# Kernel optimization log

Measured on AMD Instinct MI355X. Metric: run time of the kernel, lower is better.

Reference implementation:

```python
import jax, jax.numpy as jnp
import numpy as np

LN_EPS = 1e-5  # torch nn.LayerNorm default eps


def _layernorm(x, g, b):
    m = jnp.mean(x, -1, keepdims=True)
    v = jnp.mean((x - m) ** 2, -1, keepdims=True)
    return (x - m) / jnp.sqrt(v + LN_EPS) * g + b


def _dw_causal_conv(x, w, bias=None):
    # x: (B, L, C); w: (C, K) depthwise kernels; causal via left-pad K-1
    C = x.shape[-1]
    K = w.shape[-1]
    xt = jnp.swapaxes(x, 1, 2)                       # (B, C, L)
    xp = jnp.pad(xt, ((0, 0), (0, 0), (K - 1, 0)))
    y = jax.lax.conv_general_dilated(
        xp, w[:, None, :], (1,), 'VALID',
        feature_group_count=C, dimension_numbers=('NCH', 'OIH', 'NCH'))
    if bias is not None:
        y = y + bias[None, :, None]
    return jnp.swapaxes(y, 1, 2)                     # (B, L, C)


def _s4d(x, Bp, Cp, log_dt, Dp):
    # Diagonal SSM: kernel K[l] = sum_n C[n]*dB[n]*dA[n]^l, shared across channels
    L, Dm = x.shape[1], x.shape[2]
    n = Bp.shape[0]
    A = -jnp.arange(1, n + 1, dtype=x.dtype)
    dt = jnp.clip(jnp.exp(log_dt), 1e-4, 1.0)
    dA = jnp.exp(jnp.clip(dt * A, -10.0, 10.0))                  # (n,)
    dB = (dA - 1.0) / jnp.minimum(A, -1e-4) * Bp                 # (n,)
    pows = dA[:, None] ** jnp.arange(L, dtype=x.dtype)[None, :]  # (n, L)
    Kk = jnp.nan_to_num((Cp * dB) @ pows, nan=0.0, posinf=0.0, neginf=0.0)  # (L,)
    y = _dw_causal_conv(x, jnp.broadcast_to(Kk[None, :], (Dm, L)))
    return y + Dp * x


def _mamba_block(x, g, b, W_in, cw, cb, sB, sC, ldt, sD, W_out, rs):
    res = x
    h = _layernorm(x, g, b)
    xz = h @ W_in.T                                  # (B, L, 2*d_inner)
    xp, z = jnp.split(xz, 2, axis=-1)
    xc = _dw_causal_conv(xp, cw, cb)                 # depthwise causal conv, k=4
    y = _s4d(xc, sB, sC, ldt, sD) * jax.nn.sigmoid(z)
    y = y @ W_out.T
    return res + jnp.clip(rs, 0.0, 1.5) * y          # dropout is identity in eval


def _forward(spatial_tokens_init, pos_embed, ln_g, ln_b, W_in, conv_w, conv_b,
             ssm_B, ssm_C, log_dt, ssm_D, W_out, res_scale, fin_g, fin_b,
             imp_W1, imp_b1, imp_W2, imp_b2, tex_W, tex_b, edge_W, edge_b,
             str_W, str_b):
    x = spatial_tokens_init + pos_embed
    for i in range(ln_g.shape[0]):  # fixed small layer count
        x = _mamba_block(x, ln_g[i], ln_b[i], W_in[i], conv_w[i], conv_b[i],
                         ssm_B[i], ssm_C[i], log_dt[i], ssm_D[i], W_out[i],
                         res_scale[i])
    tokens = _layernorm(x, fin_g, fin_b)
    # F.normalize(dim=-1, eps=1e-6)
    tn = tokens / jnp.maximum(jnp.sqrt(jnp.sum(tokens ** 2, -1, keepdims=True)), 1e-6)
    h = jax.nn.gelu(tn @ imp_W1.T + imp_b1, approximate=False)
    logits = (h @ imp_W2.T + imp_b2)[..., 0]
    w = jax.nn.softmax(logits, axis=-1)
    feats = jnp.sum(tokens * w[..., None], axis=1)
    return (feats,
            feats @ tex_W.T + tex_b,
            feats @ edge_W.T + edge_b,
            feats @ str_W.T + str_b,
            tokens, w)


B, N, D, DI, NL, NS, KC, DH = 512, 256, 128, 256, 4, 16, 4, 64
H = D // 2


def setup_inputs() -> dict:
    ks = jax.random.split(jax.random.key(0), 26)
    r = lambda k, sh, s=0.02: jax.random.normal(k, sh, dtype=jnp.float32) * s
    inp = {
        'spatial_tokens_init': jax.random.normal(ks[0], (B, N, D), dtype=jnp.float32),
        'pos_embed': r(ks[1], (1, N, D)),
        'ln_g': jnp.ones((NL, D), jnp.float32),
        'ln_b': jnp.zeros((NL, D), jnp.float32),
        'W_in': r(ks[2], (NL, 2 * DI, D)),
        'conv_w': r(ks[3], (NL, DI, KC), 0.2),
        'conv_b': r(ks[4], (NL, DI), 0.02),
        'ssm_B': r(ks[5], (NL, NS)),
        'ssm_C': r(ks[6], (NL, NS)),
        'log_dt': jax.random.uniform(ks[7], (NL,), jnp.float32,
                                     minval=float(np.log(1e-3)), maxval=float(np.log(0.1))),
        'ssm_D': jnp.zeros((NL,), jnp.float32),
        'W_out': r(ks[8], (NL, D, DI)),
        'res_scale': jnp.ones((NL,), jnp.float32),
        'fin_g': jnp.ones((D,), jnp.float32),
        'fin_b': jnp.zeros((D,), jnp.float32),
        'imp_W1': r(ks[9], (H, D)),
        'imp_b1': jnp.zeros((H,), jnp.float32),
        'imp_W2': r(ks[10], (1, H)),
        'imp_b2': jnp.zeros((1,), jnp.float32),
        'tex_W': r(ks[11], (DH, D)),
        'tex_b': jnp.zeros((DH,), jnp.float32),
        'edge_W': r(ks[12], (DH, D)),
        'edge_b': jnp.zeros((DH,), jnp.float32),
        'str_W': r(ks[13], (DH, D)),
        'str_b': jnp.zeros((DH,), jnp.float32),
    }
    return inp


def reference(spatial_tokens_init, pos_embed, ln_g, ln_b, W_in, conv_w, conv_b,
              ssm_B, ssm_C, log_dt, ssm_D, W_out, res_scale, fin_g, fin_b,
              imp_W1, imp_b1, imp_W2, imp_b2, tex_W, tex_b, edge_W, edge_b,
              str_W, str_b):
    return _forward(spatial_tokens_init, pos_embed, ln_g, ln_b, W_in, conv_w,
                    conv_b, ssm_B, ssm_C, log_dt, ssm_D, W_out, res_scale,
                    fin_g, fin_b, imp_W1, imp_b1, imp_W2, imp_b2, tex_W, tex_b,
                    edge_W, edge_b, str_W, str_b)
```

## Files before the change

### kernel.cpp

```cpp
#include <hip/hip_runtime.h>
#include <hip/hip_bf16.h>


typedef __bf16 bf16_8 __attribute__((ext_vector_type(8)));
typedef __bf16 bf16_4 __attribute__((ext_vector_type(4)));
typedef float  f32_4  __attribute__((ext_vector_type(4)));

#define GLOAD16(src, dst) __builtin_amdgcn_global_load_lds( \
    (const __attribute__((address_space(1))) void*)(src),   \
    (__attribute__((address_space(3))) void*)(dst), 16, 0, 0)

__device__ __forceinline__ float fsig(float z) {
    float e = __expf(-z);
    return __builtin_amdgcn_rcpf(1.0f + e);
}

__global__ __launch_bounds__(256) void prep_kernel(const float* __restrict__ win,
                                                   const float* __restrict__ wout,
                                                   const float* __restrict__ w1,
                                                   __bf16* __restrict__ win16,
                                                   __bf16* __restrict__ wout16,
                                                   __bf16* __restrict__ w116) {
    int i = blockIdx.x * 256 + threadIdx.x;
    if (i < 4 * 512 * 128) win16[i] = (__bf16)win[i];
    if (i < 4 * 128 * 256) wout16[i] = (__bf16)wout[i];
    if (i < 64 * 128)      w116[i]  = (__bf16)w1[i];
}

__global__ __launch_bounds__(256) void build_T_kernel(const float* __restrict__ Bp,
                                                      const float* __restrict__ Cp,
                                                      const float* __restrict__ ldt,
                                                      const float* __restrict__ Dpv,
                                                      __bf16* __restrict__ Tg,
                                                      float* __restrict__ Rg) {
    __shared__ float rsum[4];
    int layer = blockIdx.y, l = blockIdx.x, j = threadIdx.x;
    int d = l - j;
    float val = 0.0f;
    if (d >= 0) {
        float dt = expf(ldt[layer]);
        dt = fminf(fmaxf(dt, 1e-4f), 1.0f);
        #pragma unroll
        for (int n = 0; n < 16; ++n) {
            float A = -(float)(n + 1);
            float e = fminf(fmaxf(dt * A, -10.0f), 10.0f);
            float dA = expf(e);
            float dB = (dA - 1.0f) / A * Bp[layer * 16 + n];
            val += Cp[layer * 16 + n] * dB * expf(e * (float)d);
        }
        if (d == 0) val += Dpv[layer];
    }
    __bf16 bv = (__bf16)val;
    Tg[layer * 65536 + l * 256 + j] = bv;
    float fv = (float)bv;
    #pragma unroll
    for (int o = 32; o; o >>= 1) fv += __shfl_xor(fv, o);
    int lane = j & 63, wave = j >> 6;
    if (lane == 0) rsum[wave] = fv;
    __syncthreads();
    if (j == 0) Rg[layer * 256 + l] = rsum[0] + rsum[1] + rsum[2] + rsum[3];
}

__global__ __launch_bounds__(256) void ln_first_kernel(const float4* __restrict__ init4,
                                                       const float4* __restrict__ pos4,
                                                       const float* __restrict__ g,
                                                       const float* __restrict__ bta,
                                                       __bf16* __restrict__ x,
                                                       __bf16* __restrict__ h) {
    int tid = threadIdx.x;
    int wave = tid >> 6, lane = tid & 63;
    int half = lane >> 5, l32 = lane & 31;
    long tok = (long)blockIdx.x * 8 + wave * 2 + half;
    float4 v = init4[tok * 32 + l32];
    float4 p = pos4[(tok & 255) * 32 + l32];
    v.x += p.x; v.y += p.y; v.z += p.z; v.w += p.w;
    int d0 = l32 * 4;
    bf16_4 xv;
    xv[0] = (__bf16)v.x; xv[1] = (__bf16)v.y; xv[2] = (__bf16)v.z; xv[3] = (__bf16)v.w;
    *(bf16_4*)(x + tok * 128 + d0) = xv;
    float s = v.x + v.y + v.z + v.w;
    float ss = v.x * v.x + v.y * v.y + v.z * v.z + v.w * v.w;
    #pragma unroll
    for (int o = 16; o; o >>= 1) { s += __shfl_xor(s, o); ss += __shfl_xor(ss, o); }
    float m = s * (1.0f / 128.0f);
    float var = ss * (1.0f / 128.0f) - m * m;
    float r = rsqrtf(var + 1e-5f);
    bf16_4 hv;
    hv[0] = (__bf16)((v.x - m) * r * g[d0]     + bta[d0]);
    hv[1] = (__bf16)((v.y - m) * r * g[d0 + 1] + bta[d0 + 1]);
    hv[2] = (__bf16)((v.z - m) * r * g[d0 + 2] + bta[d0 + 2]);
    hv[3] = (__bf16)((v.w - m) * r * g[d0 + 3] + bta[d0 + 3]);
    *(bf16_4*)(h + tok * 128 + d0) = hv;
}

__global__ __launch_bounds__(256) void gemm1_kernel(const __bf16* __restrict__ hmat,
                                                    const __bf16* __restrict__ win,
                                                    __bf16* __restrict__ xpt,
                                                    __bf16* __restrict__ z) {
    __shared__ __align__(16) __bf16 As[128 * 64];
    __shared__ __align__(16) __bf16 Bs[128 * 64];
    int tid = threadIdx.x;
    int bid = blockIdx.x;
    long m0 = (long)((bid & 7) + ((bid >> 5) << 3)) * 128;
    int n0 = ((bid >> 3) & 3) * 128;
    int wave = tid >> 6, lane = tid & 63;
    int wm = wave >> 1, wn = wave & 1;
    int lrow = lane & 15, lk = (lane >> 4) * 8;
    int r7 = lrow & 7;
    int rl = lane >> 3, sl = lane & 7;
    int scol = ((sl ^ rl) << 3);
    f32_4 acc[4][4] = {};

    for (int kc = 0; kc < 2; ++kc) {
        const __bf16* asrc = hmat + m0 * 128 + kc * 64;
        const __bf16* bsrc = win + (long)n0 * 128 + kc * 64;
        #pragma unroll
        for (int j = 0; j < 4; ++j) {
            int chunk = wave * 4 + j;
            GLOAD16(asrc + (long)(chunk * 8 + rl) * 128 + scol, As + chunk * 512);
            GLOAD16(bsrc + (long)(chunk * 8 + rl) * 128 + scol, Bs + chunk * 512);
        }
        __syncthreads();
        #pragma unroll
        for (int kk = 0; kk < 64; kk += 32) {
            int sw = ((((kk + lk) >> 3) ^ r7) << 3);
            bf16_8 a[4], b[4];
            #pragma unroll
            for (int mt = 0; mt < 4; ++mt)
                a[mt] = *(const bf16_8*)(As + (wm * 64 + mt * 16 + lrow) * 64 + sw);
            #pragma unroll
            for (int nt = 0; nt < 4; ++nt)
                b[nt] = *(const bf16_8*)(Bs + (wn * 64 + nt * 16 + lrow) * 64 + sw);
            #pragma unroll
            for (int mt = 0; mt < 4; ++mt)
                #pragma unroll
                for (int nt = 0; nt < 4; ++nt)
                    acc[mt][nt] = __builtin_amdgcn_mfma_f32_16x16x32_bf16(
                        a[mt], b[nt], acc[mt][nt], 0, 0, 0);
        }
        __syncthreads();
    }

    int row_base = (lane >> 4) * 4;
    int col = lane & 15;
    if (n0 < 256) {
        #pragma unroll
        for (int mt = 0; mt < 4; ++mt) {
            long mg = m0 + wm * 64 + mt * 16 + row_base;
            int b = (int)(mg >> 8), l = (int)(mg & 255);
            #pragma unroll
            for (int nt = 0; nt < 4; ++nt) {
                int ng = n0 + wn * 64 + nt * 16 + col;
                bf16_4 o;
                #pragma unroll
                for (int r = 0; r < 4; ++r) o[r] = (__bf16)acc[mt][nt][r];
                *(bf16_4*)(xpt + (long)b * 65536 + (long)ng * 256 + l) = o;
            }
        }
    } else {
        int ncol0 = n0 - 256;
        #pragma unroll
        for (int mt = 0; mt < 4; ++mt) {
            long mg = m0 + wm * 64 + mt * 16 + row_base;
            #pragma unroll
            for (int nt = 0; nt < 4; ++nt) {
                int ng = ncol0 + wn * 64 + nt * 16 + col;
                #pragma unroll
                for (int r = 0; r < 4; ++r)
                    z[(mg + r) * 256 + ng] = (__bf16)acc[mt][nt][r];
            }
        }
    }
}

__global__ __launch_bounds__(512) void ssm_gemm_kernel(const __bf16* __restrict__ xct,
                                                       __bf16* __restrict__ zy,
                                                       const __bf16* __restrict__ Tg,
                                                       const float* __restrict__ Rg,
                                                       const float* __restrict__ cw,
                                                       const float* __restrict__ cb) {
    __shared__ __align__(16) __bf16 As[256 * 64];
    __shared__ __align__(16) __bf16 Bs[128 * 64];
    __shared__ float  bnd[3][128];
    __shared__ float  Rs[256];
    int tid = threadIdx.x;
    int batch = blockIdx.x >> 1;
    int ntile = blockIdx.x & 1;
    int c0 = ntile * 128;

    int wave = tid >> 6, lane = tid & 63;
    int wm = wave >> 2, wn = wave & 3;
    int lrow = lane & 15, lk = (lane >> 4) * 8;
    int r7 = lrow & 7;
    int quad = lane >> 4;
    int rl = lane >> 3, sl = lane & 7;
    int scol = ((sl ^ rl) << 3);
    f32_4 acc[8][2] = {};
    const __bf16* bsrc0 = xct + (long)batch * 65536 + (long)c0 * 256;

    if (tid < 256) Rs[tid] = Rg[tid];

    for (int kc = 0; kc < 4; ++kc) {
        int j0 = kc * 64;
        const __bf16* asrc = Tg + j0;
        const __bf16* bsrc = bsrc0 + j0;
        #pragma unroll
        for (int j = 0; j < 4; ++j) {
            int chunk = wave * 4 + j;
            GLOAD16(asrc + (long)(chunk * 8 + rl) * 256 + scol, As + chunk * 512);
        }
        #pragma unroll
        for (int j = 0; j < 2; ++j) {
            int chunk = wave * 2 + j;
            GLOAD16(bsrc + (long)(chunk * 8 + rl) * 256 + scol, Bs + chunk * 512);
        }
        __syncthreads();
        #pragma unroll
        for (int kk = 0; kk < 64; kk += 32) {
            int sw = ((((kk + lk) >> 3) ^ r7) << 3);
            bf16_8 b0 = *(const bf16_8*)(Bs + (wn * 32 + lrow) * 64 + sw);
            bf16_8 b1 = *(const bf16_8*)(Bs + (wn * 32 + 16 + lrow) * 64 + sw);
            #pragma unroll
            for (int mt = 0; mt < 8; ++mt) {
                bf16_8 a = *(const bf16_8*)(As + (wm * 128 + mt * 16 + lrow) * 64 + sw);
                acc[mt][0] = __builtin_amdgcn_mfma_f32_16x16x32_bf16(a, b0, acc[mt][0], 0, 0, 0);
                acc[mt][1] = __builtin_amdgcn_mfma_f32_16x16x32_bf16(a, b1, acc[mt][1], 0, 0, 0);
            }
        }
        __syncthreads();
    }

    if (wm == 0 && quad == 3) {
        #pragma unroll
        for (int nt = 0; nt < 2; ++nt) {
            int colb = wn * 32 + nt * 16 + lrow;
            bnd[0][colb] = acc[7][nt][1];
            bnd[1][colb] = acc[7][nt][2];
            bnd[2][colb] = acc[7][nt][3];
        }
    }
    __syncthreads();

    float4 wv[2]; float cbv[2];
    #pragma unroll
    for (int nt = 0; nt < 2; ++nt) {
        int cg = c0 + wn * 32 + nt * 16 + lrow;
        wv[nt] = *(const float4*)(cw + cg * 4);
        cbv[nt] = cb[cg];
    }
    int src = (lane + 48) & 63;

    #pragma unroll
    for (int mt = 0; mt < 8; ++mt) {
        int lbase = wm * 128 + mt * 16 + quad * 4;
        int mp = mt > 0 ? mt - 1 : 0;
        float R0 = Rs[lbase], R1 = Rs[lbase + 1], R2 = Rs[lbase + 2], R3 = Rs[lbase + 3];
        #pragma unroll
        for (int nt = 0; nt < 2; ++nt) {
            int colb = wn * 32 + nt * 16 + lrow;
            int cg = c0 + colb;
            float s1 = __shfl(acc[mt][nt][3], src);
            float s2 = __shfl(acc[mt][nt][2], src);
            float s3 = __shfl(acc[mt][nt][1], src);
            float t1, t2, t3;
            if (mt == 0) {
                if (wm == 1) { t1 = bnd[2][colb]; t2 = bnd[1][colb]; t3 = bnd[0][colb]; }
                else         { t1 = 0.0f; t2 = 0.0f; t3 = 0.0f; }
            } else {
                t1 = __shfl(acc[mp][nt][3], src);
                t2 = __shfl(acc[mp][nt][2], src);
                t3 = __shfl(acc[mp][nt][1], src);
            }
            float pm1 = quad ? s1 : t1;
            float pm2 = quad ? s2 : t2;
            float pm3 = quad ? s3 : t3;
            float p0 = acc[mt][nt][0], p1 = acc[mt][nt][1];
            float p2 = acc[mt][nt][2], p3 = acc[mt][nt][3];
            float y0 = wv[nt].x * pm3 + wv[nt].y * pm2 + wv[nt].z * pm1 + wv[nt].w * p0 + cbv[nt] * R0;
            float y1 = wv[nt].x * pm2 + wv[nt].y * pm1 + wv[nt].z * p0  + wv[nt].w * p1 + cbv[nt] * R1;
            float y2 = wv[nt].x * pm1 + wv[nt].y * p0  + wv[nt].z * p1  + wv[nt].w * p2 + cbv[nt] * R2;
            float y3 = wv[nt].x * p0  + wv[nt].y * p1  + wv[nt].z * p2  + wv[nt].w * p3 + cbv[nt] * R3;
            long base = (long)batch * 65536 + (long)lbase * 256 + cg;
            float z0 = (float)zy[base];
            float z1 = (float)zy[base + 256];
            float z2 = (float)zy[base + 512];
            float z3 = (float)zy[base + 768];
            zy[base]       = (__bf16)(y0 * fsig(z0));
            zy[base + 256] = (__bf16)(y1 * fsig(z1));
            zy[base + 512] = (__bf16)(y2 * fsig(z2));
            zy[base + 768] = (__bf16)(y3 * fsig(z3));
        }
    }
}

__global__ __launch_bounds__(256) void gemm2_kernel(const __bf16* __restrict__ y,
                                                    const __bf16* __restrict__ wout,
                                                    __bf16* __restrict__ x,
                                                    const float* __restrict__ rs_p,
                                                    const float* __restrict__ g,
                                                    const float* __restrict__ bta,
                                                    __bf16* __restrict__ hout,
                                                    float* __restrict__ tokens_out,
                                                    int final_mode) {
    __shared__ __align__(16) __bf16 As[64 * 64];
    __shared__ __align__(16) __bf16 Bs[128 * 64];
    __shared__ float s_sum[64][2];
    __shared__ float s_ssq[64][2];
    int tid = threadIdx.x;
    long m0 = (long)blockIdx.x * 64;
    int wave = tid >> 6, lane = tid & 63;
    int wm = wave >> 1, wn = wave & 1;
    int lrow = lane & 15, lk = (lane >> 4) * 8;
    int r7 = lrow & 7;
    int rl = lane >> 3, sl = lane & 7;
    int scol = ((sl ^ rl) << 3);
    f32_4 acc[2][4] = {};

    for (int kc = 0; kc < 4; ++kc) {
        const __bf16* asrc = y + m0 * 256 + kc * 64;
        const __bf16* bsrc = wout + kc * 64;
        #pragma unroll
        for (int j = 0; j < 2; ++j) {
            int chunk = wave * 2 + j;
            GLOAD16(asrc + (long)(chunk * 8 + rl) * 256 + scol, As + chunk * 512);
        }
        #pragma unroll
        for (int j = 0; j < 4; ++j) {
            int chunk = wave * 4 + j;
            GLOAD16(bsrc + (long)(chunk * 8 + rl) * 256 + scol, Bs + chunk * 512);
        }
        __syncthreads();
        #pragma unroll
        for (int kk = 0; kk < 64; kk += 32) {
            int sw = ((((kk + lk) >> 3) ^ r7) << 3);
            bf16_8 a[2], b[4];
            #pragma unroll
            for (int mt = 0; mt < 2; ++mt)
                a[mt] = *(const bf16_8*)(As + (wm * 32 + mt * 16 + lrow) * 64 + sw);
            #pragma unroll
            for (int nt = 0; nt < 4; ++nt)
                b[nt] = *(const bf16_8*)(Bs + (wn * 64 + nt * 16 + lrow) * 64 + sw);
            #pragma unroll
            for (int mt = 0; mt < 2; ++mt)
                #pragma unroll
                for (int nt = 0; nt < 4; ++nt)
                    acc[mt][nt] = __builtin_amdgcn_mfma_f32_16x16x32_bf16(
                        a[mt], b[nt], acc[mt][nt], 0, 0, 0);
        }
        __syncthreads();
    }

    float rs = rs_p[0];
    rs = fminf(fmaxf(rs, 0.0f), 1.5f);
    int quad = lane >> 4;
    int col = lane & 15;

    #pragma unroll
    for (int mt = 0; mt < 2; ++mt) {
        int tb = wm * 32 + mt * 16 + quad * 4;
        long mg = m0 + tb;
        #pragma unroll
        for (int r = 0; r < 4; ++r) {
            float s = 0.0f, ss = 0.0f;
            #pragma unroll
            for (int nt = 0; nt < 4; ++nt) {
                int d = wn * 64 + nt * 16 + col;
                float xv = (float)x[(mg + r) * 128 + d] + rs * acc[mt][nt][r];
                acc[mt][nt][r] = xv;
                s += xv; ss += xv * xv;
            }
            #pragma unroll
            for (int o = 8; o; o >>= 1) { s += __shfl_xor(s, o); ss += __shfl_xor(ss, o); }
            if (col == 0) {
                s_sum[tb + r][wn] = s;
                s_ssq[tb + r][wn] = ss;
            }
        }
    }
    __syncthreads();

    #pragma unroll
    for (int mt = 0; mt < 2; ++mt) {
        int tb = wm * 32 + mt * 16 + quad * 4;
        long mg = m0 + tb;
        #pragma unroll
        for (int r = 0; r < 4; ++r) {
            float s  = s_sum[tb + r][0] + s_sum[tb + r][1];
            float ss = s_ssq[tb + r][0] + s_ssq[tb + r][1];
            float m = s * (1.0f / 128.0f);
            float var = ss * (1.0f / 128.0f) - m * m;
            float rstd = rsqrtf(var + 1e-5f);
            #pragma unroll
            for (int nt = 0; nt < 4; ++nt) {
                int d = wn * 64 + nt * 16 + col;
                float xv = acc[mt][nt][r];
                float t = (xv - m) * rstd * g[d] + bta[d];
                if (!final_mode) {
                    x[(mg + r) * 128 + d] = (__bf16)xv;
                    hout[(mg + r) * 128 + d] = (__bf16)t;
                } else {
                    tokens_out[(mg + r) * 128 + d] = t;
                }
            }
        }
    }
}

__global__ __launch_bounds__(256) void l2n_kernel(const float4* __restrict__ tokens4,
                                                  __bf16* __restrict__ tn) {
    int tid = threadIdx.x;
    int wave = tid >> 6, lane = tid & 63;
    int half = lane >> 5, l32 = lane & 31;
    long tok = (long)blockIdx.x * 8 + wave * 2 + half;
    float4 t = tokens4[tok * 32 + l32];
    float q = t.x * t.x + t.y * t.y + t.z * t.z + t.w * t.w;
    #pragma unroll
    for (int o = 16; o; o >>= 1) q += __shfl_xor(q, o);
    float inv = 1.0f / fmaxf(sqrtf(q), 1e-6f);
    bf16_4 o4;
    o4[0] = (__bf16)(t.x * inv); o4[1] = (__bf16)(t.y * inv);
    o4[2] = (__bf16)(t.z * inv); o4[3] = (__bf16)(t.w * inv);
    *(bf16_4*)(tn + tok * 128 + l32 * 4) = o4;
}

#define LDA 136
__global__ __launch_bounds__(256) void mlp_kernel(const __bf16* __restrict__ tn,
                                                  const __bf16* __restrict__ w1b,
                                                  const float* __restrict__ b1,
                                                  const float* __restrict__ W2,
                                                  const float* __restrict__ b2,
                                                  float* __restrict__ logits) {
    __shared__ __bf16 As[128 * LDA];
    __shared__ __bf16 Bs[64 * LDA];
    int tid = threadIdx.x;
    long m0 = (long)blockIdx.x * 128;
    const __bf16* asrc = tn + m0 * 128;
    #pragma unroll
    for (int i = 0; i < 8; ++i) {
        int idx = tid + i * 256;
        int row = idx >> 4, c = idx & 15;
        uint4 v = *(const uint4*)(asrc + row * 128 + c * 8);
        *(uint4*)(As + row * LDA + c * 8) = v;
    }
    #pragma unroll
    for (int i = 0; i < 4; ++i) {
        int idx = tid + i * 256;
        int row = idx >> 4, c = idx & 15;
        uint4 v = *(const uint4*)(w1b + row * 128 + c * 8);
        *(uint4*)(Bs + row * LDA + c * 8) = v;
    }
    __syncthreads();

    int wave = tid >> 6, lane = tid & 63;
    int lrow = lane & 15, lk = (lane >> 4) * 8;
    f32_4 acc[2][4] = {};
    #pragma unroll
    for (int kk = 0; kk < 128; kk += 32) {
        bf16_8 a[2], b[4];
        #pragma unroll
        for (int mt = 0; mt < 2; ++mt)
            a[mt] = *(const bf16_8*)(As + (wave * 32 + mt * 16 + lrow) * LDA + kk + lk);
        #pragma unroll
        for (int nt = 0; nt < 4; ++nt)
            b[nt] = *(const bf16_8*)(Bs + (nt * 16 + lrow) * LDA + kk + lk);
        #pragma unroll
        for (int mt = 0; mt < 2; ++mt)
            #pragma unroll
            for (int nt = 0; nt < 4; ++nt)
                acc[mt][nt] = __builtin_amdgcn_mfma_f32_16x16x32_bf16(
                    a[mt], b[nt], acc[mt][nt], 0, 0, 0);
    }

    int col = lane & 15, quad = lane >> 4;
    float b2v = b2[0];
    #pragma unroll
    for (int mt = 0; mt < 2; ++mt) {
        #pragma unroll
        for (int r = 0; r < 4; ++r) {
            float p = 0.0f;
            #pragma unroll
            for (int nt = 0; nt < 4; ++nt) {
                int jx = nt * 16 + col;
                float a = acc[mt][nt][r] + b1[jx];
                float gl = 0.5f * a * (1.0f + erff(a * 0.70710678118654752f));
                p += gl * W2[jx];
            }
            #pragma unroll
            for (int o = 8; o; o >>= 1) p += __shfl_xor(p, o);
            if (col == 0) {
                long tok = m0 + wave * 32 + mt * 16 + quad * 4 + r;
                logits[tok] = p + b2v;
            }
        }
    }
}

__global__ __launch_bounds__(256) void head_kernel(const float* __restrict__ tokens,
                                                   const float* __restrict__ logits,
                                                   const float* __restrict__ texW,
                                                   const float* __restrict__ texb,
                                                   const float* __restrict__ edgeW,
                                                   const float* __restrict__ edgeb,
                                                   const float* __restrict__ strW,
                                                   const float* __restrict__ strb,
                                                   float* __restrict__ feats_out,
                                                   float* __restrict__ tex_out,
                                                   float* __restrict__ edge_out,
                                                   float* __restrict__ str_out,
                                                   float* __restrict__ w_out) {
    __shared__ float wsm[256];
    __shared__ float red[8];
    __shared__ float feats_s[128];
    int b = blockIdx.x, tid = threadIdx.x;
    int lane = tid & 63, wave = tid >> 6;
    float lg = logits[(long)b * 256 + tid];
    float mx = lg;
    #pragma unroll
    for (int o = 32; o; o >>= 1) mx = fmaxf(mx, __shfl_xor(mx, o));
    if (lane == 0) red[wave] = mx;
    __syncthreads();
    float bm = fmaxf(fmaxf(red[0], red[1]), fmaxf(red[2], red[3]));
    float e = expf(lg - bm);
    float se = e;
    #pragma unroll
    for (int o = 32; o; o >>= 1) se += __shfl_xor(se, o);
    if (lane == 0) red[4 + wave] = se;
    __syncthreads();
    float tot = red[4] + red[5] + red[6] + red[7];
    float w = e / tot;
    wsm[tid] = w;
    w_out[(long)b * 256 + tid] = w;
    __syncthreads();
    if (tid < 128) {
        float acc = 0.0f;
        const float* tb = tokens + (long)b * 256 * 128 + tid;
        #pragma unroll 4
        for (int l = 0; l < 256; ++l) acc += tb[l * 128] * wsm[l];
        feats_s[tid] = acc;
        feats_out[(long)b * 128 + tid] = acc;
    }
    __syncthreads();
    if (tid < 192) {
        int head = tid >> 6, j = tid & 63;
        const float* W  = head == 0 ? texW : (head == 1 ? edgeW : strW);
        const float* bi = head == 0 ? texb : (head == 1 ? edgeb : strb);
        float* outp     = head == 0 ? tex_out : (head == 1 ? edge_out : str_out);
        const float* wr = W + j * 128;
        float acc = 0.0f;
        #pragma unroll 8
        for (int k = 0; k < 128; ++k) acc += feats_s[k] * wr[k];
        outp[(long)b * 64 + j] = acc + bi[j];
    }
}

extern "C" void kernel_launch(void* const* d_in, const int* in_sizes, int n_in,
                              void* d_out, int out_size, void* d_ws, size_t ws_size,
                              hipStream_t stream) {
    const float* init   = (const float*)d_in[0];
    const float* pos    = (const float*)d_in[1];
    const float* ln_g   = (const float*)d_in[2];
    const float* ln_b   = (const float*)d_in[3];
    const float* W_in   = (const float*)d_in[4];
    const float* conv_w = (const float*)d_in[5];
    const float* conv_b = (const float*)d_in[6];
    const float* ssm_B  = (const float*)d_in[7];
    const float* ssm_C  = (const float*)d_in[8];
    const float* log_dt = (const float*)d_in[9];
    const float* ssm_D  = (const float*)d_in[10];
    const float* W_out  = (const float*)d_in[11];
    const float* res_sc = (const float*)d_in[12];
    const float* fin_g  = (const float*)d_in[13];
    const float* fin_b  = (const float*)d_in[14];
    const float* imp_W1 = (const float*)d_in[15];
    const float* imp_b1 = (const float*)d_in[16];
    const float* imp_W2 = (const float*)d_in[17];
    const float* imp_b2 = (const float*)d_in[18];
    const float* tex_W  = (const float*)d_in[19];
    const float* tex_b  = (const float*)d_in[20];
    const float* edge_W = (const float*)d_in[21];
    const float* edge_b = (const float*)d_in[22];
    const float* str_W  = (const float*)d_in[23];
    const float* str_b  = (const float*)d_in[24];

    float* out = (float*)d_out;
    char* ws = (char*)d_ws;
    __bf16* x      = (__bf16*)ws;
    __bf16* xpt    = (__bf16*)(ws + 67108864);
    __bf16* zb     = (__bf16*)(ws + 134217728);
    __bf16* hb     = (__bf16*)(ws + 201326592);
    __bf16* win16  = (__bf16*)(ws + 234881024);
    __bf16* wout16 = (__bf16*)(ws + 235405312);
    float*  logits = (float*)(ws + 235667456);
    __bf16* w1b    = (__bf16*)(ws + 236191744);
    __bf16* Tg     = (__bf16*)(ws + 236208128);
    float*  Rg     = (float*)(ws + 236732416);

    float* tokens = out + 163840;

    prep_kernel<<<1024, 256, 0, stream>>>(W_in, W_out, imp_W1, win16, wout16, w1b);
    build_T_kernel<<<dim3(256, 4), 256, 0, stream>>>(ssm_B, ssm_C, log_dt, ssm_D, Tg, Rg);
    ln_first_kernel<<<16384, 256, 0, stream>>>((const float4*)init, (const float4*)pos,
                                               ln_g, ln_b, x, hb);
    for (int l = 0; l < 4; ++l) {
        gemm1_kernel<<<4096, 256, 0, stream>>>(hb, win16 + l * 65536, xpt, zb);
        ssm_gemm_kernel<<<1024, 512, 0, stream>>>(xpt, zb, Tg + l * 65536, Rg + l * 256,
                                                  conv_w + l * 1024, conv_b + l * 256);
        int fin = (l == 3);
        const float* gn = fin ? fin_g : ln_g + (l + 1) * 128;
        const float* bn = fin ? fin_b : ln_b + (l + 1) * 128;
        gemm2_kernel<<<2048, 256, 0, stream>>>(zb, wout16 + l * 32768, x, res_sc + l,
                                               gn, bn, hb, fin ? tokens : nullptr, fin);
    }
    __bf16* tn = hb;
    l2n_kernel<<<16384, 256, 0, stream>>>((const float4*)tokens, tn);
    mlp_kernel<<<1024, 256, 0, stream>>>(tn, w1b, imp_b1, imp_W2, imp_b2, logits);
    head_kernel<<<512, 256, 0, stream>>>(tokens, logits, tex_W, tex_b, edge_W, edge_b,
                                         str_W, str_b, out, out + 65536, out + 98304,
                                         out + 131072, out + 16941056);
}
```

Before: 697.8 us.

## Compute z gate inside SSM kernel instead of materializing it in gemm1

Gemm1 now produces only the xp half of the input projection. The SSM kernel recomputes the z half for its own 256x128 tile with an extra MFMA pass over h and W_in, and keeps it in registers. The sigmoid gating then reads z directly from those accumulators. This removes the z write and read round-trip through global memory and halves the gemm1 grid. The cost is an additional 16x2 accumulator array in the SSM kernel, which raises register pressure and may reduce occupancy.

```diff
diff --git a/kernel.cpp b/kernel.cpp
--- a/kernel.cpp
+++ b/kernel.cpp
@@ -95,14 +95,13 @@
 
 __global__ __launch_bounds__(256) void gemm1_kernel(const __bf16* __restrict__ hmat,
                                                     const __bf16* __restrict__ win,
-                                                    __bf16* __restrict__ xpt,
-                                                    __bf16* __restrict__ z) {
+                                                    __bf16* __restrict__ xpt) {
     __shared__ __align__(16) __bf16 As[128 * 64];
     __shared__ __align__(16) __bf16 Bs[128 * 64];
     int tid = threadIdx.x;
     int bid = blockIdx.x;
-    long m0 = (long)((bid & 7) + ((bid >> 5) << 3)) * 128;
-    int n0 = ((bid >> 3) & 3) * 128;
+    long m0 = (long)((bid & 7) + ((bid >> 4) << 3)) * 128;
+    int n0 = ((bid >> 3) & 1) * 128;
     int wave = tid >> 6, lane = tid & 63;
     int wm = wave >> 1, wn = wave & 1;
     int lrow = lane & 15, lk = (lane >> 4) * 8;
@@ -143,38 +142,25 @@
 
     int row_base = (lane >> 4) * 4;
     int col = lane & 15;
-    if (n0 < 256) {
-        #pragma unroll
-        for (int mt = 0; mt < 4; ++mt) {
-            long mg = m0 + wm * 64 + mt * 16 + row_base;
-            int b = (int)(mg >> 8), l = (int)(mg & 255);
-            #pragma unroll
-            for (int nt = 0; nt < 4; ++nt) {
-                int ng = n0 + wn * 64 + nt * 16 + col;
-                bf16_4 o;
-                #pragma unroll
-                for (int r = 0; r < 4; ++r) o[r] = (__bf16)acc[mt][nt][r];
-                *(bf16_4*)(xpt + (long)b * 65536 + (long)ng * 256 + l) = o;
-            }
-        }
-    } else {
-        int ncol0 = n0 - 256;
-        #pragma unroll
-        for (int mt = 0; mt < 4; ++mt) {
-            long mg = m0 + wm * 64 + mt * 16 + row_base;
-            #pragma unroll
-            for (int nt = 0; nt < 4; ++nt) {
-                int ng = ncol0 + wn * 64 + nt * 16 + col;
-                #pragma unroll
-                for (int r = 0; r < 4; ++r)
-                    z[(mg + r) * 256 + ng] = (__bf16)acc[mt][nt][r];
-            }
+    #pragma unroll
+    for (int mt = 0; mt < 4; ++mt) {
+        long mg = m0 + wm * 64 + mt * 16 + row_base;
+        int b = (int)(mg >> 8), l = (int)(mg & 255);
+        #pragma unroll
+        for (int nt = 0; nt < 4; ++nt) {
+            int ng = n0 + wn * 64 + nt * 16 + col;
+            bf16_4 o;
+            #pragma unroll
+            for (int r = 0; r < 4; ++r) o[r] = (__bf16)acc[mt][nt][r];
+            *(bf16_4*)(xpt + (long)b * 65536 + (long)ng * 256 + l) = o;
         }
     }
 }
 
 __global__ __launch_bounds__(512) void ssm_gemm_kernel(const __bf16* __restrict__ xct,
-                                                       __bf16* __restrict__ zy,
+                                                       const __bf16* __restrict__ hmat,
+                                                       const __bf16* __restrict__ winz,
+                                                       __bf16* __restrict__ yb,
                                                        const __bf16* __restrict__ Tg,
                                                        const float* __restrict__ Rg,
                                                        const float* __restrict__ cw,
@@ -196,10 +182,40 @@
     int rl = lane >> 3, sl = lane & 7;
     int scol = ((sl ^ rl) << 3);
     f32_4 acc[8][2] = {};
+    f32_4 accz[8][2] = {};
+
+    if (tid < 256) Rs[tid] = Rg[tid];
+
+    const __bf16* hsrc0 = hmat + (long)batch * 32768;
+    for (int kc = 0; kc < 2; ++kc) {
+        int j0 = kc * 64;
+        #pragma unroll
+        for (int j = 0; j < 4; ++j) {
+            int chunk = wave * 4 + j;
+            GLOAD16(hsrc0 + (long)(chunk * 8 + rl) * 128 + j0 + scol, As + chunk * 512);
+        }
+        #pragma unroll
+        for (int j = 0; j < 2; ++j) {
+            int chunk = wave * 2 + j;
+            GLOAD16(winz + (long)(c0 + chunk * 8 + rl) * 128 + j0 + scol, Bs + chunk * 512);
+        }
+        __syncthreads();
+        #pragma unroll
+        for (int kk = 0; kk < 64; kk += 32) {
+            int sw = ((((kk + lk) >> 3) ^ r7) << 3);
+            bf16_8 b0 = *(const bf16_8*)(Bs + (wn * 32 + lrow) * 64 + sw);
+            bf16_8 b1 = *(const bf16_8*)(Bs + (wn * 32 + 16 + lrow) * 64 + sw);
+            #pragma unroll
+            for (int mt = 0; mt < 8; ++mt) {
+                bf16_8 a = *(const bf16_8*)(As + (wm * 128 + mt * 16 + lrow) * 64 + sw);
+                accz[mt][0] = __builtin_amdgcn_mfma_f32_16x16x32_bf16(a, b0, accz[mt][0], 0, 0, 0);
+                accz[mt][1] = __builtin_amdgcn_mfma_f32_16x16x32_bf16(a, b1, accz[mt][1], 0, 0, 0);
+            }
+        }
+        __syncthreads();
+    }
+
     const __bf16* bsrc0 = xct + (long)batch * 65536 + (long)c0 * 256;
-
-    if (tid < 256) Rs[tid] = Rg[tid];
-
     for (int kc = 0; kc < 4; ++kc) {
         int j0 = kc * 64;
         const __bf16* asrc = Tg + j0;
@@ -281,14 +297,10 @@
             float y2 = wv[nt].x * pm1 + wv[nt].y * p0  + wv[nt].z * p1  + wv[nt].w * p2 + cbv[nt] * R2;
             float y3 = wv[nt].x * p0  + wv[nt].y * p1  + wv[nt].z * p2  + wv[nt].w * p3 + cbv[nt] * R3;
             long base = (long)batch * 65536 + (long)lbase * 256 + cg;
-            float z0 = (float)zy[base];
-            float z1 = (float)zy[base + 256];
-            float z2 = (float)zy[base + 512];
-            float z3 = (float)zy[base + 768];
-            zy[base]       = (__bf16)(y0 * fsig(z0));
-            zy[base + 256] = (__bf16)(y1 * fsig(z1));
-            zy[base + 512] = (__bf16)(y2 * fsig(z2));
-            zy[base + 768] = (__bf16)(y3 * fsig(z3));
+            yb[base]       = (__bf16)(y0 * fsig(accz[mt][nt][0]));
+            yb[base + 256] = (__bf16)(y1 * fsig(accz[mt][nt][1]));
+            yb[base + 512] = (__bf16)(y2 * fsig(accz[mt][nt][2]));
+            yb[base + 768] = (__bf16)(y3 * fsig(accz[mt][nt][3]));
         }
     }
 }
@@ -586,7 +598,7 @@
     char* ws = (char*)d_ws;
     __bf16* x      = (__bf16*)ws;
     __bf16* xpt    = (__bf16*)(ws + 67108864);
-    __bf16* zb     = (__bf16*)(ws + 134217728);
+    __bf16* yb     = (__bf16*)(ws + 134217728);
     __bf16* hb     = (__bf16*)(ws + 201326592);
     __bf16* win16  = (__bf16*)(ws + 234881024);
     __bf16* wout16 = (__bf16*)(ws + 235405312);
@@ -602,13 +614,14 @@
     ln_first_kernel<<<16384, 256, 0, stream>>>((const float4*)init, (const float4*)pos,
                                                ln_g, ln_b, x, hb);
     for (int l = 0; l < 4; ++l) {
-        gemm1_kernel<<<4096, 256, 0, stream>>>(hb, win16 + l * 65536, xpt, zb);
-        ssm_gemm_kernel<<<1024, 512, 0, stream>>>(xpt, zb, Tg + l * 65536, Rg + l * 256,
+        gemm1_kernel<<<2048, 256, 0, stream>>>(hb, win16 + l * 65536, xpt);
+        ssm_gemm_kernel<<<1024, 512, 0, stream>>>(xpt, hb, win16 + l * 65536 + 32768,
+                                                  yb, Tg + l * 65536, Rg + l * 256,
                                                   conv_w + l * 1024, conv_b + l * 256);
         int fin = (l == 3);
         const float* gn = fin ? fin_g : ln_g + (l + 1) * 128;
         const float* bn = fin ? fin_b : ln_b + (l + 1) * 128;
-        gemm2_kernel<<<2048, 256, 0, stream>>>(zb, wout16 + l * 32768, x, res_sc + l,
+        gemm2_kernel<<<2048, 256, 0, stream>>>(yb, wout16 + l * 32768, x, res_sc + l,
                                                gn, bn, hb, fin ? tokens : nullptr, fin);
     }
     __bf16* tn = hb;
```

Result: no change. 699.6 us (+0.3%).
